# Performance work log

Measured on AMD Instinct MI355X. Metric: run time of the kernel, lower is better.

## Reference

```python
import jax, jax.numpy as jnp
import numpy as np

D_MODEL = 1024
NUM_HEADS = 16
HEAD_DIM = D_MODEL // NUM_HEADS
B, S = 2, 2048


def setup_inputs() -> dict:
    key = jax.random.key(0)
    ks = jax.random.split(key, 11)
    scale = 1.0 / np.sqrt(D_MODEL)
    inp = {
        "Q": jax.random.normal(ks[0], (B, S, D_MODEL), jnp.float32),
        "K": jax.random.normal(ks[1], (B, S, D_MODEL), jnp.float32),
        "V": jax.random.normal(ks[2], (B, S, D_MODEL), jnp.float32),
        # Linear weights stored as [in, out] (transposed nn.Linear layout)
        "Wq": jax.random.normal(ks[3], (D_MODEL, D_MODEL), jnp.float32) * scale,
        "bq": jax.random.normal(ks[4], (D_MODEL,), jnp.float32) * scale,
        "Wk": jax.random.normal(ks[5], (D_MODEL, D_MODEL), jnp.float32) * scale,
        "bk": jax.random.normal(ks[6], (D_MODEL,), jnp.float32) * scale,
        "Wv": jax.random.normal(ks[7], (D_MODEL, D_MODEL), jnp.float32) * scale,
        "bv": jax.random.normal(ks[8], (D_MODEL,), jnp.float32) * scale,
        "Wo": jax.random.normal(ks[9], (D_MODEL, D_MODEL), jnp.float32) * scale,
        "bo": jax.random.normal(ks[10], (D_MODEL,), jnp.float32) * scale,
    }
    return inp


def _split_heads(x):
    # [B, S, D] -> [B, H, S, Dh]
    b, s, _ = x.shape
    return x.reshape(b, s, NUM_HEADS, HEAD_DIM).transpose(0, 2, 1, 3)


def reference(Q, K, V, Wq, bq, Wk, bk, Wv, bv, Wo, bo):
    q = _split_heads(Q @ Wq + bq)   # [B,H,S,Dh]
    k = _split_heads(K @ Wk + bk)
    v = _split_heads(V @ Wv + bv)
    scores = jnp.einsum("bhqd,bhkd->bhqk", q, k) / jnp.sqrt(
        jnp.asarray(HEAD_DIM, q.dtype))
    attn = jax.nn.softmax(scores, axis=-1)
    out = jnp.einsum("bhqk,bhkd->bhqd", attn, v)  # [B,H,S,Dh]
    out = out.transpose(0, 2, 1, 3).reshape(Q.shape[0], -1, D_MODEL)
    return out @ Wo + bo
```

## Files before the change

kernel.cpp:

```cpp
#include <hip/hip_runtime.h>
#include <hip/hip_bf16.h>

typedef short bf16x4 __attribute__((ext_vector_type(4)));
typedef short bf16x8 __attribute__((ext_vector_type(8)));
typedef float fp32x4 __attribute__((ext_vector_type(4)));

#define MFMA16(a, b, c) __builtin_amdgcn_mfma_f32_16x16x32_bf16(a, b, c, 0, 0, 0)

static __device__ __forceinline__ short f2bf(float f) {
    unsigned int b = __float_as_uint(f);
    b += 0x7fffu + ((b >> 16) & 1u);
    return (short)(b >> 16);
}

static __device__ __forceinline__ unsigned int cvt_pk_bf16(float lo, float hi) {
    unsigned int r;
    asm("v_cvt_pk_bf16_f32 %0, %1, %2" : "=v"(r) : "v"(lo), "v"(hi));
    return r;
}

static __device__ __forceinline__ void gload_lds16(const void* g, void* l) {
    __builtin_amdgcn_global_load_lds(
        (const __attribute__((address_space(1))) unsigned int*)g,
        (__attribute__((address_space(3))) unsigned int*)l, 16, 0, 0);
}

typedef unsigned int uint2v __attribute__((ext_vector_type(2)));

__global__ __launch_bounds__(256) void transpose_w(
    const float* __restrict__ W0, const float* __restrict__ W1,
    const float* __restrict__ W2, const float* __restrict__ W3,
    short* __restrict__ wbt)
{
    __shared__ short t[64][68];
    const int tid = threadIdx.x;
    const int z = blockIdx.z;
    const float* W = (z == 0) ? W0 : (z == 1) ? W1 : (z == 2) ? W2 : W3;
    short* dst = wbt + (size_t)z * 1024 * 1024;
    const int k0 = blockIdx.x * 64, n0 = blockIdx.y * 64;

#pragma unroll
    for (int p = 0; p < 4; ++p) {
        int c = p * 256 + tid;
        int kr = c >> 4, seg = c & 15;
        fp32x4 f = *(const fp32x4*)&W[(k0 + kr) * 1024 + n0 + seg * 4];
        uint2v u;
        u.x = cvt_pk_bf16(f[0], f[1]);
        u.y = cvt_pk_bf16(f[2], f[3]);
        *(uint2v*)&t[kr][seg * 4] = u;
    }
    __syncthreads();
#pragma unroll
    for (int p = 0; p < 2; ++p) {
        int c = p * 256 + tid;
        int nr = c >> 3, ks = c & 7;
        bf16x8 v;
#pragma unroll
        for (int i = 0; i < 8; ++i) v[i] = t[ks * 8 + i][nr];
        *(bf16x8*)&dst[(n0 + nr) * 1024 + k0 + ks * 8] = v;
    }
}

__global__ __launch_bounds__(256) void convert_x(
    const float* __restrict__ Q, const float* __restrict__ K,
    const float* __restrict__ V,
    short* __restrict__ xq, short* __restrict__ xk, short* __restrict__ xv)
{
    const int z = blockIdx.y;
    const float* src = (z == 0) ? Q : (z == 1) ? K : V;
    short* dst = (z == 0) ? xq : (z == 1) ? xk : xv;
    const int idx = blockIdx.x * 256 + threadIdx.x;
#pragma unroll
    for (int it = 0; it < 4; ++it) {
        size_t base = ((size_t)it * 131072 + idx) * 8;
        fp32x4 a = *(const fp32x4*)&src[base];
        fp32x4 b = *(const fp32x4*)&src[base + 4];
        uint2v u0, u1;
        u0.x = cvt_pk_bf16(a[0], a[1]);
        u0.y = cvt_pk_bf16(a[2], a[3]);
        u1.x = cvt_pk_bf16(b[0], b[1]);
        u1.y = cvt_pk_bf16(b[2], b[3]);
        *(uint2v*)&dst[base] = u0;
        *(uint2v*)&dst[base + 4] = u1;
    }
}

struct GemmArgs {
    const void* X[3];
    const short* W;
    const float* bias[3];
    void* out[3];
};

template <bool XFP32, bool HEADED>
__global__ __launch_bounds__(256) void gemm128(GemmArgs ga)
{
    __shared__ __align__(16) short lds_a[128 * 40];
    __shared__ __align__(16) short lds_b[128 * 32];

    const int tid  = threadIdx.x;
    const int lane = tid & 63;
    const int wv   = tid >> 6;
    const int l15  = lane & 15;
    const int quad = lane >> 4;
    const int wm   = (wv >> 1) * 64;
    const int wn   = (wv & 1) * 64;
    const int sread = (quad ^ ((l15 >> 1) & 3)) * 8;

    const int nwg = gridDim.x * gridDim.y * gridDim.z;
    const int lid = blockIdx.x + gridDim.x * (blockIdx.y + gridDim.y * blockIdx.z);
    const int swz = (lid & 7) * (nwg >> 3) + (lid >> 3);
    const int z   = swz >> 8;
    const int rem = swz & 255;
    const int m0  = (rem >> 3) * 128;
    const int n0  = (rem & 7) * 128;

    const void*  Xv   = ga.X[z];
    const short* W    = ga.W + (size_t)z * 1024 * 1024;
    const float* bias = ga.bias[z];
    void* outv        = ga.out[z];

    fp32x4 acc[4][4];
#pragma unroll
    for (int i = 0; i < 4; ++i)
#pragma unroll
        for (int j = 0; j < 4; ++j)
#pragma unroll
            for (int r = 0; r < 4; ++r) acc[i][j][r] = 0.f;

    for (int k0 = 0; k0 < 1024; k0 += 32) {
        __syncthreads();
        if (XFP32) {
            const float* X = (const float*)Xv;
#pragma unroll
            for (int p = 0; p < 4; ++p) {
                int c = p * 256 + tid;
                int row = c >> 3, ks = c & 7;
                fp32x4 f = *(const fp32x4*)&X[(m0 + row) * 1024 + k0 + ks * 4];
                uint2v u;
                u.x = cvt_pk_bf16(f[0], f[1]);
                u.y = cvt_pk_bf16(f[2], f[3]);
                *(uint2v*)&lds_a[row * 40 + ks * 4] = u;
            }
        } else {
            const short* X = (const short*)Xv;
#pragma unroll
            for (int p = 0; p < 2; ++p) {
                int c = p * 256 + tid;
                int row = c >> 2, s = c & 3;
                int sc = s ^ ((row >> 1) & 3);
                gload_lds16(&X[(m0 + row) * 1024 + k0 + sc * 8],
                            &lds_a[(p * 256 + wv * 64) * 8]);
            }
        }
#pragma unroll
        for (int p = 0; p < 2; ++p) {
            int c = p * 256 + tid;
            int row = c >> 2, s = c & 3;
            int sc = s ^ ((row >> 1) & 3);
            gload_lds16(&W[(n0 + row) * 1024 + k0 + sc * 8],
                        &lds_b[(p * 256 + wv * 64) * 8]);
        }
        __syncthreads();

        bf16x8 af[4], bf[4];
#pragma unroll
        for (int i = 0; i < 4; ++i)
            af[i] = XFP32
                ? *(bf16x8*)&lds_a[(wm + i * 16 + l15) * 40 + quad * 8]
                : *(bf16x8*)&lds_a[(wm + i * 16 + l15) * 32 + sread];
#pragma unroll
        for (int j = 0; j < 4; ++j)
            bf[j] = *(bf16x8*)&lds_b[(wn + j * 16 + l15) * 32 + sread];
#pragma unroll
        for (int i = 0; i < 4; ++i)
#pragma unroll
            for (int j = 0; j < 4; ++j)
                acc[i][j] = MFMA16(af[i], bf[j], acc[i][j]);
    }

#pragma unroll
    for (int i = 0; i < 4; ++i)
#pragma unroll
        for (int j = 0; j < 4; ++j)
#pragma unroll
            for (int r = 0; r < 4; ++r) {
                int row = m0 + wm + i * 16 + quad * 4 + r;
                int col = n0 + wn + j * 16 + l15;
                float v = acc[i][j][r] + bias[col];
                if (HEADED) {
                    int b = row >> 11, s = row & 2047;
                    int h = col >> 6,  dh = col & 63;
                    ((short*)outv)[(((b * 16) + h) * 2048 + s) * 64 + dh] = f2bf(v);
                } else {
                    ((float*)outv)[row * 1024 + col] = v;
                }
            }
}

__global__ __launch_bounds__(256) void attention128(
    const short* __restrict__ q, const short* __restrict__ k,
    const short* __restrict__ v, short* __restrict__ ctx)
{
    __shared__ __align__(16) short lds_k[64 * 64];
    __shared__ __align__(16) short lds_vt[64 * 74];

    const int tid  = threadIdx.x;
    const int lane = tid & 63;
    const int wv   = tid >> 6;
    const int l15  = lane & 15;
    const int quad = lane >> 4;
    const int bh   = blockIdx.y;
    const int q0   = blockIdx.x * 128 + wv * 32;

    const short* qb = q + (size_t)bh * 2048 * 64;
    const short* kb = k + (size_t)bh * 2048 * 64;
    const short* vb = v + (size_t)bh * 2048 * 64;

    bf16x8 qf[2][2];
#pragma unroll
    for (int qt = 0; qt < 2; ++qt)
#pragma unroll
        for (int h2 = 0; h2 < 2; ++h2)
            qf[qt][h2] = *(const bf16x8*)
                &qb[(q0 + qt * 16 + l15) * 64 + h2 * 32 + quad * 8];

    fp32x4 O[2][4];
    fp32x4 rs4[2];
#pragma unroll
    for (int qt = 0; qt < 2; ++qt) {
#pragma unroll
        for (int g = 0; g < 4; ++g)
#pragma unroll
            for (int r = 0; r < 4; ++r) O[qt][g][r] = 0.f;
#pragma unroll
        for (int r = 0; r < 4; ++r) rs4[qt][r] = 0.f;
    }

    const float SCL2E = 0.125f * 1.44269504088896340736f;

    const int k2   = tid >> 3;
    const int seg  = tid & 7;
    const int kk0  = k2 * 2;
    const int pos0 = (kk0 & 32) + (((kk0 & 15) >> 2) << 3)
                   + (((kk0 >> 4) & 1) << 2) + (kk0 & 3);

    const int ksrc  = ((lane & 7) ^ (lane >> 3)) * 8;
    const int krowl = lane >> 3;
    const int kswz  = l15 & 7;

    for (int key0 = 0; key0 < 2048; key0 += 64) {
        __syncthreads();
        bf16x8 v0 = *(const bf16x8*)&vb[(key0 + kk0) * 64 + seg * 8];
        bf16x8 v1 = *(const bf16x8*)&vb[(key0 + kk0 + 1) * 64 + seg * 8];
#pragma unroll
        for (int p = 0; p < 2; ++p) {
            int row = p * 32 + wv * 8 + krowl;
            gload_lds16(&kb[(key0 + row) * 64 + ksrc],
                        &lds_k[(p * 32 + wv * 8) * 64]);
        }
#pragma unroll
        for (int i = 0; i < 8; ++i) {
            unsigned int w = (unsigned int)(unsigned short)v0[i]
                           | ((unsigned int)(unsigned short)v1[i] << 16);
            *(unsigned int*)&lds_vt[(seg * 8 + i) * 74 + pos0] = w;
        }
        __syncthreads();

        bf16x8 kf[4][2];
#pragma unroll
        for (int kc = 0; kc < 4; ++kc)
#pragma unroll
            for (int h2 = 0; h2 < 2; ++h2)
                kf[kc][h2] = *(bf16x8*)
                    &lds_k[(kc * 16 + l15) * 64 + (((h2 * 4 + quad) ^ kswz) * 8)];

        union { bf16x8 v; unsigned int u[4]; } pfr[2][2];
#pragma unroll
        for (int qt = 0; qt < 2; ++qt) {
#pragma unroll
            for (int kc = 0; kc < 4; ++kc) {
                fp32x4 s;
#pragma unroll
                for (int r = 0; r < 4; ++r) s[r] = 0.f;
                s = MFMA16(kf[kc][0], qf[qt][0], s);
                s = MFMA16(kf[kc][1], qf[qt][1], s);
                fp32x4 p;
#pragma unroll
                for (int r = 0; r < 4; ++r) {
                    p[r] = __builtin_amdgcn_exp2f(s[r] * SCL2E);
                    rs4[qt][r] += p[r];
                }
                pfr[qt][kc >> 1].u[(kc & 1) * 2 + 0] = cvt_pk_bf16(p[0], p[1]);
                pfr[qt][kc >> 1].u[(kc & 1) * 2 + 1] = cvt_pk_bf16(p[2], p[3]);
            }
        }

#pragma unroll
        for (int g = 0; g < 4; ++g)
#pragma unroll
            for (int ks = 0; ks < 2; ++ks) {
                bf16x8 vf = *(bf16x8*)
                    &lds_vt[(g * 16 + l15) * 74 + ks * 32 + quad * 8];
#pragma unroll
                for (int qt = 0; qt < 2; ++qt)
                    O[qt][g] = MFMA16(pfr[qt][ks].v, vf, O[qt][g]);
            }
    }

    const int b = bh >> 4, h = bh & 15;
#pragma unroll
    for (int qt = 0; qt < 2; ++qt) {
        float t = (rs4[qt][0] + rs4[qt][1]) + (rs4[qt][2] + rs4[qt][3]);
        t += __shfl_xor(t, 16);
        t += __shfl_xor(t, 32);
#pragma unroll
        for (int r = 0; r < 4; ++r) {
            float tot = __shfl(t, quad * 4 + r);
            float inv = 1.f / tot;
            int qq  = q0 + qt * 16 + quad * 4 + r;
            int row = b * 2048 + qq;
#pragma unroll
            for (int g = 0; g < 4; ++g) {
                int col = h * 64 + g * 16 + l15;
                ctx[row * 1024 + col] = f2bf(O[qt][g][r] * inv);
            }
        }
    }
}

extern "C" void kernel_launch(void* const* d_in, const int* in_sizes, int n_in,
                              void* d_out, int out_size, void* d_ws, size_t ws_size,
                              hipStream_t stream) {
    const float* Q  = (const float*)d_in[0];
    const float* K  = (const float*)d_in[1];
    const float* V  = (const float*)d_in[2];
    const float* Wq = (const float*)d_in[3];
    const float* bq = (const float*)d_in[4];
    const float* Wk = (const float*)d_in[5];
    const float* bk = (const float*)d_in[6];
    const float* Wv = (const float*)d_in[7];
    const float* bv = (const float*)d_in[8];
    const float* Wo = (const float*)d_in[9];
    const float* bo = (const float*)d_in[10];

    const size_t NEL = 4096ull * 1024ull;
    short* wbt  = (short*)d_ws;
    short* vbuf = wbt + 4 * 1024 * 1024;
    short* cbuf = vbuf + NEL;
    short* xq   = cbuf + NEL;
    short* xk   = xq + NEL;
    short* xv   = cbuf;
    short* qbuf = (short*)d_out;
    short* kbuf = (short*)d_out + NEL;

    const bool big_ws = ws_size >= (40ull << 20);

    dim3 blk(256);
    hipLaunchKernelGGL(transpose_w, dim3(16, 16, 4), blk, 0, stream,
                       Wq, Wk, Wv, Wo, wbt);

    GemmArgs g1;
    g1.W = wbt;
    g1.bias[0] = bq; g1.bias[1] = bk; g1.bias[2] = bv;
    g1.out[0] = qbuf; g1.out[1] = kbuf; g1.out[2] = vbuf;
    if (big_ws) {
        hipLaunchKernelGGL(convert_x, dim3(512, 3), blk, 0, stream,
                           Q, K, V, xq, xk, xv);
        g1.X[0] = xq; g1.X[1] = xk; g1.X[2] = xv;
        hipLaunchKernelGGL((gemm128<false, true>), dim3(8, 32, 3), blk, 0,
                           stream, g1);
    } else {
        g1.X[0] = Q;  g1.X[1] = K;  g1.X[2] = V;
        hipLaunchKernelGGL((gemm128<true, true>), dim3(8, 32, 3), blk, 0,
                           stream, g1);
    }

    hipLaunchKernelGGL(attention128, dim3(16, 32), blk, 0, stream,
                       qbuf, kbuf, vbuf, cbuf);

    GemmArgs g2;
    g2.X[0] = cbuf; g2.X[1] = cbuf; g2.X[2] = cbuf;
    g2.W = wbt + 3ull * 1024 * 1024;
    g2.bias[0] = bo; g2.bias[1] = bo; g2.bias[2] = bo;
    g2.out[0] = d_out; g2.out[1] = d_out; g2.out[2] = d_out;
    hipLaunchKernelGGL((gemm128<false, false>), dim3(8, 32, 1), blk, 0, stream, g2);
}
```

Measured before the change: 232.4 us.

## Merge weight transpose and input conversion into one prepass; permute P-fragment key ordering

Combines the weight transpose/convert kernel and the activation fp32-to-bf16 kernel into a single launch whose block index picks the job. This removes one kernel launch and lets both jobs share the GPU at once. Separately, the attention kernel changes the key-position permutation used when staging V into LDS and the matching half-swap of the packed P fragment, which changes the LDS write pattern, probably to cut bank conflicts. The permutation must stay consistent between the V staging and the P packing, or the result will be wrong.

After: 251.9 us. 1.08x slower.

```diff
diff --git a/kernel.cpp b/kernel.cpp
--- a/kernel.cpp
+++ b/kernel.cpp
@@ -27,61 +27,64 @@
 
 typedef unsigned int uint2v __attribute__((ext_vector_type(2)));
 
-__global__ __launch_bounds__(256) void transpose_w(
+__global__ __launch_bounds__(256) void prepass(
     const float* __restrict__ W0, const float* __restrict__ W1,
     const float* __restrict__ W2, const float* __restrict__ W3,
-    short* __restrict__ wbt)
-{
-    __shared__ short t[64][68];
-    const int tid = threadIdx.x;
-    const int z = blockIdx.z;
-    const float* W = (z == 0) ? W0 : (z == 1) ? W1 : (z == 2) ? W2 : W3;
-    short* dst = wbt + (size_t)z * 1024 * 1024;
-    const int k0 = blockIdx.x * 64, n0 = blockIdx.y * 64;
-
-#pragma unroll
-    for (int p = 0; p < 4; ++p) {
-        int c = p * 256 + tid;
-        int kr = c >> 4, seg = c & 15;
-        fp32x4 f = *(const fp32x4*)&W[(k0 + kr) * 1024 + n0 + seg * 4];
-        uint2v u;
-        u.x = cvt_pk_bf16(f[0], f[1]);
-        u.y = cvt_pk_bf16(f[2], f[3]);
-        *(uint2v*)&t[kr][seg * 4] = u;
-    }
-    __syncthreads();
-#pragma unroll
-    for (int p = 0; p < 2; ++p) {
-        int c = p * 256 + tid;
-        int nr = c >> 3, ks = c & 7;
-        bf16x8 v;
-#pragma unroll
-        for (int i = 0; i < 8; ++i) v[i] = t[ks * 8 + i][nr];
-        *(bf16x8*)&dst[(n0 + nr) * 1024 + k0 + ks * 8] = v;
-    }
-}
-
-__global__ __launch_bounds__(256) void convert_x(
+    short* __restrict__ wbt,
     const float* __restrict__ Q, const float* __restrict__ K,
     const float* __restrict__ V,
     short* __restrict__ xq, short* __restrict__ xk, short* __restrict__ xv)
 {
-    const int z = blockIdx.y;
-    const float* src = (z == 0) ? Q : (z == 1) ? K : V;
-    short* dst = (z == 0) ? xq : (z == 1) ? xk : xv;
-    const int idx = blockIdx.x * 256 + threadIdx.x;
-#pragma unroll
-    for (int it = 0; it < 4; ++it) {
-        size_t base = ((size_t)it * 131072 + idx) * 8;
-        fp32x4 a = *(const fp32x4*)&src[base];
-        fp32x4 b = *(const fp32x4*)&src[base + 4];
-        uint2v u0, u1;
-        u0.x = cvt_pk_bf16(a[0], a[1]);
-        u0.y = cvt_pk_bf16(a[2], a[3]);
-        u1.x = cvt_pk_bf16(b[0], b[1]);
-        u1.y = cvt_pk_bf16(b[2], b[3]);
-        *(uint2v*)&dst[base] = u0;
-        *(uint2v*)&dst[base + 4] = u1;
+    __shared__ short t[64][68];
+    const int tid = threadIdx.x;
+    const int b   = blockIdx.x;
+
+    if (b < 1024) {
+        const int z = b >> 8;
+        const float* W = (z == 0) ? W0 : (z == 1) ? W1 : (z == 2) ? W2 : W3;
+        short* dst = wbt + (size_t)z * 1024 * 1024;
+        const int k0 = (b & 15) * 64, n0 = ((b >> 4) & 15) * 64;
+
+#pragma unroll
+        for (int p = 0; p < 4; ++p) {
+            int c = p * 256 + tid;
+            int kr = c >> 4, seg = c & 15;
+            fp32x4 f = *(const fp32x4*)&W[(k0 + kr) * 1024 + n0 + seg * 4];
+            uint2v u;
+            u.x = cvt_pk_bf16(f[0], f[1]);
+            u.y = cvt_pk_bf16(f[2], f[3]);
+            *(uint2v*)&t[kr][seg * 4] = u;
+        }
+        __syncthreads();
+#pragma unroll
+        for (int p = 0; p < 2; ++p) {
+            int c = p * 256 + tid;
+            int nr = c >> 3, ks = c & 7;
+            bf16x8 v;
+#pragma unroll
+            for (int i = 0; i < 8; ++i) v[i] = t[ks * 8 + i][nr];
+            *(bf16x8*)&dst[(n0 + nr) * 1024 + k0 + ks * 8] = v;
+        }
+    } else {
+        const int c = b - 1024;
+        const int z = c >> 9;
+        const int x = c & 511;
+        const float* src = (z == 0) ? Q : (z == 1) ? K : V;
+        short* dst = (z == 0) ? xq : (z == 1) ? xk : xv;
+        const int idx = x * 256 + tid;
+#pragma unroll
+        for (int it = 0; it < 4; ++it) {
+            size_t base = ((size_t)it * 131072 + idx) * 8;
+            fp32x4 a = *(const fp32x4*)&src[base];
+            fp32x4 bb = *(const fp32x4*)&src[base + 4];
+            uint2v u0, u1;
+            u0.x = cvt_pk_bf16(a[0], a[1]);
+            u0.y = cvt_pk_bf16(a[2], a[3]);
+            u1.x = cvt_pk_bf16(bb[0], bb[1]);
+            u1.y = cvt_pk_bf16(bb[2], bb[3]);
+            *(uint2v*)&dst[base] = u0;
+            *(uint2v*)&dst[base + 4] = u1;
+        }
     }
 }
 
@@ -242,8 +245,13 @@
     const int k2   = tid >> 3;
     const int seg  = tid & 7;
     const int kk0  = k2 * 2;
-    const int pos0 = (kk0 & 32) + (((kk0 & 15) >> 2) << 3)
-                   + (((kk0 >> 4) & 1) << 2) + (kk0 & 3);
+    const int q_   = (k2 & 7) >> 1;
+    const int tq_  = (q_ ^ (q_ >> 1)) & 1;
+    const int hi_  = (k2 >> 3) & 1;
+    const int pos0 = ((k2 >> 4) << 5) + (q_ << 3)
+                   + ((tq_ ^ hi_) << 2) + ((k2 & 1) << 1);
+
+    const int tq   = (quad ^ (quad >> 1)) & 1;
 
     const int ksrc  = ((lane & 7) ^ (lane >> 3)) * 8;
     const int krowl = lane >> 3;
@@ -291,8 +299,9 @@
                     p[r] = __builtin_amdgcn_exp2f(s[r] * SCL2E);
                     rs4[qt][r] += p[r];
                 }
-                pfr[qt][kc >> 1].u[(kc & 1) * 2 + 0] = cvt_pk_bf16(p[0], p[1]);
-                pfr[qt][kc >> 1].u[(kc & 1) * 2 + 1] = cvt_pk_bf16(p[2], p[3]);
+                const int h = ((kc & 1) ^ tq) << 1;
+                pfr[qt][kc >> 1].u[h]     = cvt_pk_bf16(p[0], p[1]);
+                pfr[qt][kc >> 1].u[h + 1] = cvt_pk_bf16(p[2], p[3]);
             }
         }
 
@@ -357,20 +366,20 @@
     const bool big_ws = ws_size >= (40ull << 20);
 
     dim3 blk(256);
-    hipLaunchKernelGGL(transpose_w, dim3(16, 16, 4), blk, 0, stream,
-                       Wq, Wk, Wv, Wo, wbt);
 
     GemmArgs g1;
     g1.W = wbt;
     g1.bias[0] = bq; g1.bias[1] = bk; g1.bias[2] = bv;
     g1.out[0] = qbuf; g1.out[1] = kbuf; g1.out[2] = vbuf;
     if (big_ws) {
-        hipLaunchKernelGGL(convert_x, dim3(512, 3), blk, 0, stream,
-                           Q, K, V, xq, xk, xv);
+        hipLaunchKernelGGL(prepass, dim3(2560), blk, 0, stream,
+                           Wq, Wk, Wv, Wo, wbt, Q, K, V, xq, xk, xv);
         g1.X[0] = xq; g1.X[1] = xk; g1.X[2] = xv;
         hipLaunchKernelGGL((gemm128<false, true>), dim3(8, 32, 3), blk, 0,
                            stream, g1);
     } else {
+        hipLaunchKernelGGL(prepass, dim3(1024), blk, 0, stream,
+                           Wq, Wk, Wv, Wo, wbt, Q, K, V, xq, xk, xv);
         g1.X[0] = Q;  g1.X[1] = K;  g1.X[2] = V;
         hipLaunchKernelGGL((gemm128<true, true>), dim3(8, 32, 3), blk, 0,
                            stream, g1);
```
